# Kernel tuning notes

Measured on AMD Instinct MI355X. Metric: run time of the kernel, lower is better.

## Reference

```python
import jax, jax.numpy as jnp
import numpy as np

WS, SHIFT = 4, 2
Z, H, W = 16, 32, 32
C, HEADS, MLP = 384, 12, 1536
B = 4
N = WS ** 3                      # tokens per 3D window = 64
NW = (Z // WS) * (H // WS) * (W // WS)  # windows per sample = 256
L = Z * H * W
HEAD_DIM = C // HEADS


def _rel_pos_index():
    # replicates meshgrid_3d (which reverses its args) + index arithmetic
    arrs = (np.arange(WS), np.arange(WS), np.arange(WS))  # already symmetric (cubic)
    grids = []
    for i in range(3):
        slc = [1, 1, 1]; slc[i] = WS
        a = arrs[i].reshape(slc)
        for j in range(3):
            if j != i:
                a = a.repeat(WS, axis=j)
        grids.append(a)
    coords = np.stack(grids).reshape(3, -1)            # [3, N]
    rel = coords[:, :, None] - coords[:, None, :]      # [3, N, N]
    rel = rel.transpose(1, 2, 0)                       # [N, N, 3]
    rel[:, :, 0] += WS - 1
    rel[:, :, 1] += WS - 1
    rel[:, :, 2] += WS - 1
    rel[:, :, 0] *= (2 * WS - 1) * (2 * WS - 1)
    rel[:, :, 1] *= 2 * WS - 1
    return rel.sum(-1)                                 # [N, N] ints in [0, (2ws-1)^3)


def _attn_mask():
    # shifted-window mask, exactly as in build()
    m = np.zeros((Z, H, W))
    sl = (slice(0, -WS), slice(-WS, -SHIFT), slice(-SHIFT, None))
    cnt = 0
    for z in sl:
        for h in sl:
            for w in sl:
                m[z, h, w] = cnt
                cnt += 1
    mw = m.reshape(Z // WS, WS, H // WS, WS, W // WS, WS)
    mw = mw.transpose(0, 2, 4, 1, 3, 5).reshape(-1, N)        # [nW, N]
    diff = mw[:, None, :] - mw[:, :, None]                    # [nW, N, N]
    return np.where(diff != 0, -100.0, 0.0).astype(np.float32)


REL_IDX = jnp.asarray(_rel_pos_index())
MASK = jnp.asarray(_attn_mask())


def _ln(x, g, b):
    mu = jnp.mean(x, -1, keepdims=True)
    var = jnp.mean((x - mu) ** 2, -1, keepdims=True)
    return (x - mu) / jnp.sqrt(var + 1e-5) * g + b


def setup_inputs() -> dict:
    key = jax.random.key(0)
    ks = jax.random.split(key, 16)
    s = 0.02
    return {
        "x": jax.random.normal(ks[0], (B, L, C), jnp.float32),
        "norm1_g": jnp.ones((C,), jnp.float32),
        "norm1_b": jnp.zeros((C,), jnp.float32),
        "qkv_w": jax.random.normal(ks[1], (C, 3 * C), jnp.float32) * s,
        "qkv_b": jnp.zeros((3 * C,), jnp.float32),
        "proj_w": jax.random.normal(ks[2], (C, C), jnp.float32) * s,
        "proj_b": jnp.zeros((C,), jnp.float32),
        "rel_bias": jax.random.normal(ks[3], ((2 * WS - 1) ** 3, HEADS), jnp.float32) * s,
        "norm2_g": jnp.ones((C,), jnp.float32),
        "norm2_b": jnp.zeros((C,), jnp.float32),
        "fc1_w": jax.random.normal(ks[4], (C, MLP), jnp.float32) * s,
        "fc1_b": jnp.zeros((MLP,), jnp.float32),
        "fc2_w": jax.random.normal(ks[5], (MLP, C), jnp.float32) * s,
        "fc2_b": jnp.zeros((C,), jnp.float32),
    }


def reference(x, norm1_g, norm1_b, qkv_w, qkv_b, proj_w, proj_b, rel_bias,
              norm2_g, norm2_b, fc1_w, fc1_b, fc2_w, fc2_b):
    b = x.shape[0]
    skip = x
    h = _ln(x, norm1_g, norm1_b).reshape(b, Z, H, W, C)
    h = jnp.roll(h, (-SHIFT, -SHIFT, -SHIFT), axis=(1, 2, 3))
    # window partition -> [b*nW, N, C]
    win = h.reshape(b, Z // WS, WS, H // WS, WS, W // WS, WS, C)
    win = win.transpose(0, 1, 3, 5, 2, 4, 6, 7).reshape(-1, N, C)
    # windowed multi-head attention
    qkv = (win @ qkv_w + qkv_b).reshape(-1, N, 3, HEADS, HEAD_DIM)
    qkv = qkv.transpose(2, 0, 3, 1, 4)                        # [3, bnW, h, N, d]
    q, k, v = qkv[0], qkv[1], qkv[2]
    scale = HEAD_DIM ** -0.5
    attn = jnp.einsum('whnd,whmd->whnm', q * scale, k)        # [bnW, h, N, N]
    bias = rel_bias[REL_IDX.reshape(-1)].reshape(N, N, HEADS).transpose(2, 0, 1)
    attn = attn + bias[None]
    attn = attn.reshape(b, NW, HEADS, N, N) + MASK[None, :, None]
    attn = jax.nn.softmax(attn, axis=-1).reshape(-1, HEADS, N, N)
    o = jnp.einsum('whnm,whmd->whnd', attn, v)
    o = o.transpose(0, 2, 1, 3).reshape(-1, N, C) @ proj_w + proj_b
    # window reverse + unshift
    o = o.reshape(b, Z // WS, H // WS, W // WS, WS, WS, WS, C)
    o = o.transpose(0, 1, 4, 2, 5, 3, 6, 7).reshape(b, Z, H, W, C)
    o = jnp.roll(o, (SHIFT, SHIFT, SHIFT), axis=(1, 2, 3)).reshape(b, L, C)
    x2 = skip + o
    m = _ln(x2, norm2_g, norm2_b)
    m = jax.nn.gelu(m @ fc1_w + fc1_b, approximate=False) @ fc2_w + fc2_b
    return x2 + m
```

## Files before the change

kernel.cpp:

```cpp
#include <hip/hip_runtime.h>
#include <hip/hip_bf16.h>
#include <cstdint>
#include <cmath>


typedef __attribute__((ext_vector_type(4))) float f32x4;
typedef __attribute__((ext_vector_type(8))) __bf16 bf16x8_t;

static __device__ __forceinline__ short f2bf(float f) {
  unsigned u = __builtin_bit_cast(unsigned, f);
  unsigned lsb = (u >> 16) & 1u;
  u += 0x7fffu + lsb;
  return (short)(u >> 16);
}

static __device__ __forceinline__ void gload_lds16(const short* g, short* l) {
  __builtin_amdgcn_global_load_lds(
      (const __attribute__((address_space(1))) void*)g,
      (__attribute__((address_space(3))) void*)l, 16, 0, 0);
}

static constexpr size_t OFF_Q    = 0;
static constexpr size_t OFF_K    = 50331648;
static constexpr size_t OFF_V    = 100663296;
static constexpr size_t OFF_HID  = 0;
static constexpr size_t OFF_WIN  = 201326592;
static constexpr size_t OFF_WQ   = OFF_WIN + 50331648;
static constexpr size_t OFF_WP   = OFF_WQ  + 884736;
static constexpr size_t OFF_W1   = OFF_WP  + 294912;
static constexpr size_t OFF_W2   = OFF_W1  + 1179648;

__global__ void k_w2bf_t(const float* __restrict__ w, short* __restrict__ wt,
                         int K, int N) {
  int idx = blockIdx.x * 256 + threadIdx.x;
  if (idx >= K * N) return;
  int k = idx / N, n = idx - k * N;
  wt[(size_t)n * K + k] = f2bf(w[idx]);
}

__global__ __launch_bounds__(256) void k_ln1_window(
    const float* __restrict__ x, const float* __restrict__ gw,
    const float* __restrict__ gb, short* __restrict__ win) {
  int slot = blockIdx.x * 4 + (threadIdx.x >> 6);
  int lane = threadIdx.x & 63;
  int widx = slot >> 6, n = slot & 63;
  int bidx = widx >> 8, wloc = widx & 255;
  int z = ((wloc >> 6) << 2) + (n >> 4);
  int h = (((wloc >> 3) & 7) << 2) + ((n >> 2) & 3);
  int w = ((wloc & 7) << 2) + (n & 3);
  int zs = (z + 2) & 15, hs = (h + 2) & 31, ws = (w + 2) & 31;
  const float* xp = x + ((size_t)bidx * 16384 + zs * 1024 + hs * 32 + ws) * 384;
  float2 u[3]; float s = 0.f, s2 = 0.f;
#pragma unroll
  for (int j = 0; j < 3; j++) {
    u[j] = *(const float2*)(xp + lane * 2 + j * 128);
    s += u[j].x + u[j].y; s2 += u[j].x * u[j].x + u[j].y * u[j].y;
  }
#pragma unroll
  for (int o = 1; o < 64; o <<= 1) { s += __shfl_xor(s, o); s2 += __shfl_xor(s2, o); }
  float mu = s * (1.f / 384.f);
  float rinv = rsqrtf(s2 * (1.f / 384.f) - mu * mu + 1e-5f);
  short* wp = win + (size_t)slot * 384;
#pragma unroll
  for (int j = 0; j < 3; j++) {
    int c = lane * 2 + j * 128;
    ushort2 o;
    o.x = (unsigned short)f2bf((u[j].x - mu) * rinv * gw[c] + gb[c]);
    o.y = (unsigned short)f2bf((u[j].y - mu) * rinv * gw[c + 1] + gb[c + 1]);
    *(ushort2*)(wp + c) = o;
  }
}

__global__ __launch_bounds__(256) void k_ln2(
    const float* __restrict__ x2, const float* __restrict__ gw,
    const float* __restrict__ gb, short* __restrict__ h2) {
  int t = blockIdx.x * 4 + (threadIdx.x >> 6);
  int lane = threadIdx.x & 63;
  const float* xp = x2 + (size_t)t * 384;
  float2 u[3]; float s = 0.f, s2 = 0.f;
#pragma unroll
  for (int j = 0; j < 3; j++) {
    u[j] = *(const float2*)(xp + lane * 2 + j * 128);
    s += u[j].x + u[j].y; s2 += u[j].x * u[j].x + u[j].y * u[j].y;
  }
#pragma unroll
  for (int o = 1; o < 64; o <<= 1) { s += __shfl_xor(s, o); s2 += __shfl_xor(s2, o); }
  float mu = s * (1.f / 384.f);
  float rinv = rsqrtf(s2 * (1.f / 384.f) - mu * mu + 1e-5f);
  short* hp = h2 + (size_t)t * 384;
#pragma unroll
  for (int j = 0; j < 3; j++) {
    int c = lane * 2 + j * 128;
    ushort2 o;
    o.x = (unsigned short)f2bf((u[j].x - mu) * rinv * gw[c] + gb[c]);
    o.y = (unsigned short)f2bf((u[j].y - mu) * rinv * gw[c + 1] + gb[c + 1]);
    *(ushort2*)(hp + c) = o;
  }
}

template <int EPI, int KDIM>
__global__ __launch_bounds__(256, 2) void k_gemm(
    const short* __restrict__ A, const short* __restrict__ Bt,
    const float* __restrict__ bias, short* __restrict__ ob0,
    short* __restrict__ ob1, short* __restrict__ ob2,
    const float* __restrict__ aux, float* __restrict__ of32) {
  __shared__ short As[24576];
  __shared__ short Bs[12288];
  const int tid = threadIdx.x;
  const int wave = tid >> 6, lane = tid & 63;
  const int g = lane >> 4, li = lane & 15;

  const int nx = gridDim.x;
  const int nwg = nx * gridDim.y;
  int bid = blockIdx.y * nx + blockIdx.x;
  const int cpx = nwg >> 3;
  bid = (bid & 7) * cpx + (bid >> 3);
  const int m0 = (bid / nx) << 8, n0 = (bid % nx) << 7;

  const int u_ = tid >> 3;
  const int s_ = tid & 7;
  const int sx = s_ ^ (u_ & 7);
  const int srow = (u_ << 1) + (sx >> 2);
  const int scol = (sx & 3) << 3;
  const short* gAs = A + (size_t)(m0 + srow) * KDIM + scol;
  const short* gBs = Bt + (size_t)(n0 + srow) * KDIM + scol;
  short* lAs = As + wave * 512;
  short* lBs = Bs + wave * 512;

  const int wm = wave >> 1, wn = wave & 1;
  const int li2 = li >> 1;
  const int slot = (((li & 1) << 2) + g) ^ li2;
  const int abase = wm * 4096 + li2 * 64 + slot * 8;
  const int bbase = wn * 2048 + li2 * 64 + slot * 8;

  f32x4 acc[8][4] = {};

#define STAGE(buf, kt)                                                        \
  do {                                                                        \
    _Pragma("unroll") for (int p = 0; p < 4; p++)                             \
        gload_lds16(gAs + (size_t)(p * 64) * KDIM + (kt),                     \
                    lAs + (buf) * 8192 + p * 2048);                           \
    _Pragma("unroll") for (int p = 0; p < 2; p++)                             \
        gload_lds16(gBs + (size_t)(p * 64) * KDIM + (kt),                     \
                    lBs + (buf) * 4096 + p * 2048);                           \
  } while (0)

#define COMPUTE(buf)                                                          \
  do {                                                                        \
    const short* pa = As + (buf) * 8192 + abase;                              \
    const short* pb = Bs + (buf) * 4096 + bbase;                              \
    bf16x8_t a[8], b[4];                                                      \
    _Pragma("unroll") for (int mi = 0; mi < 8; mi++)                          \
        a[mi] = *(const bf16x8_t*)(pa + mi * 512);                            \
    _Pragma("unroll") for (int ni = 0; ni < 4; ni++)                          \
        b[ni] = *(const bf16x8_t*)(pb + ni * 512);                            \
    _Pragma("unroll") for (int mi = 0; mi < 8; mi++)                          \
        _Pragma("unroll") for (int ni = 0; ni < 4; ni++) acc[mi][ni] =        \
        __builtin_amdgcn_mfma_f32_16x16x32_bf16(a[mi], b[ni], acc[mi][ni],    \
                                                0, 0, 0);                     \
  } while (0)

  constexpr int NT = KDIM / 32;
  STAGE(0, 0);
  STAGE(1, 32);
#pragma unroll 3
  for (int t = 0; t < NT; ++t) {
    asm volatile("s_waitcnt lgkmcnt(0)" ::: "memory");
    __builtin_amdgcn_s_barrier();
    if (t + 2 < NT) {
      STAGE((t + 2) % 3, (t + 2) * 32);
      asm volatile("s_waitcnt vmcnt(12)" ::: "memory");
    } else if (t + 1 < NT) {
      asm volatile("s_waitcnt vmcnt(6)" ::: "memory");
    } else {
      asm volatile("s_waitcnt vmcnt(0)" ::: "memory");
    }
    __builtin_amdgcn_s_barrier();
    COMPUTE(t % 3);
  }
#undef STAGE
#undef COMPUTE

#pragma unroll
  for (int mi = 0; mi < 8; mi++) {
#pragma unroll
    for (int ni = 0; ni < 4; ni++) {
      const int col = n0 + wn * 64 + ni * 16 + li;
      const float bc = bias[col];
      const int rbase = m0 + wm * 128 + mi * 16 + g * 4;
      if constexpr (EPI == 0) {
        const int s = col / 384;
        const int rem = col - s * 384;
        const int head = rem >> 5, d = rem & 31;
#pragma unroll
        for (int r = 0; r < 4; r++) {
          const int row = rbase + r;
          const int widx = row >> 6, n = row & 63;
          float v = acc[mi][ni][r] + bc;
          if (s == 0)
            ob0[(((size_t)widx * 12 + head) * 64 + n) * 32 + d] =
                f2bf(v * 0.17677669529663687f);
          else if (s == 1)
            ob1[(((size_t)widx * 12 + head) * 64 + n) * 32 + d] = f2bf(v);
          else
            ob2[(((size_t)widx * 12 + head) * 32 + d) * 64 + n] = f2bf(v);
        }
      } else if constexpr (EPI == 1) {
#pragma unroll
        for (int r = 0; r < 4; r++) {
          const int row = rbase + r;
          const int widx = row >> 6, n = row & 63;
          const int wloc = widx & 255, bb = widx >> 8;
          const int z = ((wloc >> 6) << 2) + (n >> 4);
          const int h = (((wloc >> 3) & 7) << 2) + ((n >> 2) & 3);
          const int w = ((wloc & 7) << 2) + (n & 3);
          const int zs = (z + 2) & 15, hs = (h + 2) & 31, wsx = (w + 2) & 31;
          const size_t t = (size_t)bb * 16384 + zs * 1024 + hs * 32 + wsx;
          of32[t * 384 + col] = aux[t * 384 + col] + acc[mi][ni][r] + bc;
        }
      } else if constexpr (EPI == 2) {
#pragma unroll
        for (int r = 0; r < 4; r++) {
          const int row = rbase + r;
          float v = acc[mi][ni][r] + bc;
          ob0[(size_t)row * 1536 + col] =
              f2bf(0.5f * v * (1.f + erff(v * 0.70710678118654752f)));
        }
      } else {
#pragma unroll
        for (int r = 0; r < 4; r++) {
          const int row = rbase + r;
          of32[(size_t)row * 384 + col] =
              aux[(size_t)row * 384 + col] + acc[mi][ni][r] + bc;
        }
      }
    }
  }
}

__global__ __launch_bounds__(256) void k_attn(
    const short* __restrict__ qb, const short* __restrict__ kb,
    const short* __restrict__ vb, const float* __restrict__ relb,
    short* __restrict__ owin) {
  __shared__ short pt[4][5120];
  const int wave = threadIdx.x >> 6;
  const int wh_ = blockIdx.x * 4 + wave;
  const int widx = wh_ / 12, head = wh_ - widx * 12;
  const int lane = threadIdx.x & 63;
  const int g = lane >> 4, li = lane & 15;
  const short* qp = qb + (size_t)wh_ * 2048;
  const short* kp = kb + (size_t)wh_ * 2048;
  const short* vp = vb + (size_t)wh_ * 2048;
  short* ptw = pt[wave];
  bf16x8_t kf[4], qf[4];
#pragma unroll
  for (int t = 0; t < 4; t++) {
    kf[t] = *(const bf16x8_t*)(kp + (t * 16 + li) * 32 + g * 8);
    qf[t] = *(const bf16x8_t*)(qp + (t * 16 + li) * 32 + g * 8);
  }
  f32x4 zero = {0.f, 0.f, 0.f, 0.f};
  f32x4 st[4][4];
#pragma unroll
  for (int ti = 0; ti < 4; ti++)
#pragma unroll
    for (int tj = 0; tj < 4; tj++)
      st[ti][tj] = __builtin_amdgcn_mfma_f32_16x16x32_bf16(kf[ti], qf[tj], zero, 0, 0, 0);
  const int wloc = widx & 255;
  const int wz = wloc >> 6, wh2 = (wloc >> 3) & 7, ww2 = wloc & 7;
#pragma unroll
  for (int tj = 0; tj < 4; tj++) {
    const int qn = tj * 16 + li;
    const int qz = qn >> 4, qh = (qn >> 2) & 3, qw = qn & 3;
    const int cq = ((wz < 3) ? 0 : ((qz < 2) ? 1 : 2)) * 9 +
                   ((wh2 < 7) ? 0 : ((qh < 2) ? 1 : 2)) * 3 +
                   ((ww2 < 7) ? 0 : ((qw < 2) ? 1 : 2));
    float mx = -1e30f;
#pragma unroll
    for (int ti = 0; ti < 4; ti++) {
#pragma unroll
      for (int r = 0; r < 4; r++) {
        const int kn = ti * 16 + g * 4 + r;
        const int kz = kn >> 4, kh = (kn >> 2) & 3, kw = kn & 3;
        const int ck = ((wz < 3) ? 0 : ((kz < 2) ? 1 : 2)) * 9 +
                       ((wh2 < 7) ? 0 : ((kh < 2) ? 1 : 2)) * 3 +
                       ((ww2 < 7) ? 0 : ((kw < 2) ? 1 : 2));
        const int idx = (qz - kz + 3) * 49 + (qh - kh + 3) * 7 + (qw - kw + 3);
        float v = st[ti][tj][r] + relb[idx * 12 + head] + ((ck == cq) ? 0.f : -100.f);
        st[ti][tj][r] = v;
        mx = fmaxf(mx, v);
      }
    }
    mx = fmaxf(mx, __shfl_xor(mx, 16));
    mx = fmaxf(mx, __shfl_xor(mx, 32));
    float sum = 0.f;
#pragma unroll
    for (int ti = 0; ti < 4; ti++)
#pragma unroll
      for (int r = 0; r < 4; r++) {
        float e = __expf(st[ti][tj][r] - mx);
        st[ti][tj][r] = e;
        sum += e;
      }
    sum += __shfl_xor(sum, 16);
    sum += __shfl_xor(sum, 32);
    const float rs = 1.f / sum;
#pragma unroll
    for (int ti = 0; ti < 4; ti++)
#pragma unroll
      for (int r = 0; r < 4; r++)
        ptw[qn * 80 + ti * 16 + g * 4 + r] = f2bf(st[ti][tj][r] * rs);
  }
  __syncthreads();
  f32x4 o[4][2] = {};
#pragma unroll
  for (int kb2 = 0; kb2 < 2; kb2++) {
    bf16x8_t pa[4], bv[2];
#pragma unroll
    for (int tq = 0; tq < 4; tq++)
      pa[tq] = *(const bf16x8_t*)(ptw + (tq * 16 + li) * 80 + kb2 * 32 + g * 8);
#pragma unroll
    for (int td = 0; td < 2; td++)
      bv[td] = *(const bf16x8_t*)(vp + (td * 16 + li) * 64 + kb2 * 32 + g * 8);
#pragma unroll
    for (int tq = 0; tq < 4; tq++)
#pragma unroll
      for (int td = 0; td < 2; td++)
        o[tq][td] = __builtin_amdgcn_mfma_f32_16x16x32_bf16(pa[tq], bv[td], o[tq][td], 0, 0, 0);
  }
#pragma unroll
  for (int tq = 0; tq < 4; tq++)
#pragma unroll
    for (int td = 0; td < 2; td++)
#pragma unroll
      for (int r = 0; r < 4; r++) {
        const int qn = tq * 16 + g * 4 + r;
        const int d = td * 16 + li;
        owin[((size_t)widx * 64 + qn) * 384 + head * 32 + d] = f2bf(o[tq][td][r]);
      }
}

extern "C" void kernel_launch(void* const* d_in, const int* in_sizes, int n_in,
                              void* d_out, int out_size, void* d_ws,
                              size_t ws_size, hipStream_t stream) {
  (void)in_sizes; (void)n_in; (void)out_size; (void)ws_size;
  const float* x      = (const float*)d_in[0];
  const float* n1g    = (const float*)d_in[1];
  const float* n1b    = (const float*)d_in[2];
  const float* qkv_w  = (const float*)d_in[3];
  const float* qkv_b  = (const float*)d_in[4];
  const float* proj_w = (const float*)d_in[5];
  const float* proj_b = (const float*)d_in[6];
  const float* relb   = (const float*)d_in[7];
  const float* n2g    = (const float*)d_in[8];
  const float* n2b    = (const float*)d_in[9];
  const float* fc1_w  = (const float*)d_in[10];
  const float* fc1_b  = (const float*)d_in[11];
  const float* fc2_w  = (const float*)d_in[12];
  const float* fc2_b  = (const float*)d_in[13];
  float* out = (float*)d_out;
  char* ws = (char*)d_ws;

  short* qbuf = (short*)(ws + OFF_Q);
  short* kbuf = (short*)(ws + OFF_K);
  short* vbuf = (short*)(ws + OFF_V);
  short* hid  = (short*)(ws + OFF_HID);
  short* win  = (short*)(ws + OFF_WIN);
  short* owin = (short*)(ws + OFF_WIN);
  short* h2   = (short*)(ws + OFF_WIN);
  float* x2   = out;
  short* wq   = (short*)(ws + OFF_WQ);
  short* wp   = (short*)(ws + OFF_WP);
  short* w1   = (short*)(ws + OFF_W1);
  short* w2   = (short*)(ws + OFF_W2);

  k_w2bf_t<<<(384 * 1152 + 255) / 256, 256, 0, stream>>>(qkv_w, wq, 384, 1152);
  k_w2bf_t<<<(384 * 384 + 255) / 256, 256, 0, stream>>>(proj_w, wp, 384, 384);
  k_w2bf_t<<<(384 * 1536 + 255) / 256, 256, 0, stream>>>(fc1_w, w1, 384, 1536);
  k_w2bf_t<<<(1536 * 384 + 255) / 256, 256, 0, stream>>>(fc2_w, w2, 1536, 384);

  k_ln1_window<<<16384, 256, 0, stream>>>(x, n1g, n1b, win);
  k_gemm<0, 384><<<dim3(9, 256), 256, 0, stream>>>(win, wq, qkv_b, qbuf, kbuf,
                                                   vbuf, nullptr, nullptr);
  k_attn<<<3072, 256, 0, stream>>>(qbuf, kbuf, vbuf, relb, owin);
  k_gemm<1, 384><<<dim3(3, 256), 256, 0, stream>>>(owin, wp, proj_b, nullptr,
                                                   nullptr, nullptr, x, x2);
  k_ln2<<<16384, 256, 0, stream>>>(x2, n2g, n2b, h2);
  k_gemm<2, 384><<<dim3(12, 256), 256, 0, stream>>>(h2, w1, fc1_b, hid, nullptr,
                                                    nullptr, nullptr, nullptr);
  k_gemm<3, 1536><<<dim3(3, 256), 256, 0, stream>>>(hid, w2, fc2_b, nullptr,
                                                    nullptr, nullptr, x2, out);
}
```

Measured before the change: 799.0 us.

## Stage QKV and FC1 epilogues through swizzled LDS for vectorized stores; tanh GELU

For the QKV projection and FC1 GEMMs, the epilogue now writes bf16 results into a swizzled shared-memory tile and then emits coalesced 16-byte global stores, instead of scattered 2-byte stores into head-major and transposed-V layouts. The aim is to cut uncoalesced write traffic. FC1's exact erf GELU is replaced by a tanh approximation computed with __expf, which changes numerics slightly. The extra LDS pass adds two barriers and reuses the A/B staging buffers.

```diff
diff --git a/kernel.cpp b/kernel.cpp
--- a/kernel.cpp
+++ b/kernel.cpp
@@ -5,6 +5,7 @@
 
 
 typedef __attribute__((ext_vector_type(4))) float f32x4;
+typedef __attribute__((ext_vector_type(4))) int i32x4;
 typedef __attribute__((ext_vector_type(8))) __bf16 bf16x8_t;
 
 static __device__ __forceinline__ short f2bf(float f) {
@@ -12,6 +13,13 @@
   unsigned lsb = (u >> 16) & 1u;
   u += 0x7fffu + lsb;
   return (short)(u >> 16);
+}
+
+static __device__ __forceinline__ float fgelu(float x) {
+  float u = 0.7978845608028654f * x * (1.f + 0.044715f * x * x);
+  float e = __expf(2.f * u);
+  float t = 1.f - 2.f / (e + 1.f);
+  return 0.5f * x * (1.f + t);
 }
 
 static __device__ __forceinline__ void gload_lds16(const short* g, short* l) {
@@ -104,8 +112,9 @@
     const float* __restrict__ bias, short* __restrict__ ob0,
     short* __restrict__ ob1, short* __restrict__ ob2,
     const float* __restrict__ aux, float* __restrict__ of32) {
-  __shared__ short As[24576];
-  __shared__ short Bs[12288];
+  __shared__ short smem[36864];
+  short* As = smem;
+  short* Bs = smem + 24576;
   const int tid = threadIdx.x;
   const int wave = tid >> 6, lane = tid & 63;
   const int g = lane >> 4, li = lane & 15;
@@ -181,57 +190,102 @@
 #undef STAGE
 #undef COMPUTE
 
-#pragma unroll
-  for (int mi = 0; mi < 8; mi++) {
-#pragma unroll
-    for (int ni = 0; ni < 4; ni++) {
-      const int col = n0 + wn * 64 + ni * 16 + li;
-      const float bc = bias[col];
-      const int rbase = m0 + wm * 128 + mi * 16 + g * 4;
-      if constexpr (EPI == 0) {
-        const int s = col / 384;
-        const int rem = col - s * 384;
-        const int head = rem >> 5, d = rem & 31;
+  if constexpr (EPI == 0 || EPI == 2) {
+    __syncthreads();
+    short* ct = smem;
+    const int s = (EPI == 0) ? (n0 / 384) : 0;
+    const float scale =
+        (EPI == 0 && s == 0) ? 0.17677669529663687f : 1.f;
+#pragma unroll
+    for (int mi = 0; mi < 8; mi++) {
+#pragma unroll
+      for (int ni = 0; ni < 4; ni++) {
+        const int colc = wn * 64 + ni * 16 + li;
+        const float bc = bias[n0 + colc];
 #pragma unroll
         for (int r = 0; r < 4; r++) {
-          const int row = rbase + r;
-          const int widx = row >> 6, n = row & 63;
+          const int row = wm * 128 + mi * 16 + g * 4 + r;
           float v = acc[mi][ni][r] + bc;
-          if (s == 0)
-            ob0[(((size_t)widx * 12 + head) * 64 + n) * 32 + d] =
-                f2bf(v * 0.17677669529663687f);
-          else if (s == 1)
-            ob1[(((size_t)widx * 12 + head) * 64 + n) * 32 + d] = f2bf(v);
-          else
-            ob2[(((size_t)widx * 12 + head) * 32 + d) * 64 + n] = f2bf(v);
+          int idx16, sub;
+          if constexpr (EPI == 0) {
+            const int hh = colc >> 5, d = colc & 31;
+            const int widx_l = row >> 6, n = row & 63;
+            const int run = widx_l * 4 + hh;
+            if (s < 2) {
+              idx16 = run * 256 + n * 4 + (d >> 3);
+              idx16 ^= (idx16 >> 4) & 7;
+              sub = d & 7;
+            } else {
+              idx16 = run * 256 + d * 8 + (n >> 3);
+              idx16 ^= (idx16 >> 3) & 7;
+              sub = n & 7;
+            }
+            v *= scale;
+          } else {
+            idx16 = row * 16 + (colc >> 3);
+            idx16 ^= (idx16 >> 4) & 7;
+            sub = colc & 7;
+            v = fgelu(v);
+          }
+          ct[idx16 * 8 + sub] = f2bf(v);
         }
-      } else if constexpr (EPI == 1) {
-#pragma unroll
-        for (int r = 0; r < 4; r++) {
-          const int row = rbase + r;
-          const int widx = row >> 6, n = row & 63;
-          const int wloc = widx & 255, bb = widx >> 8;
-          const int z = ((wloc >> 6) << 2) + (n >> 4);
-          const int h = (((wloc >> 3) & 7) << 2) + ((n >> 2) & 3);
-          const int w = ((wloc & 7) << 2) + (n & 3);
-          const int zs = (z + 2) & 15, hs = (h + 2) & 31, wsx = (w + 2) & 31;
-          const size_t t = (size_t)bb * 16384 + zs * 1024 + hs * 32 + wsx;
-          of32[t * 384 + col] = aux[t * 384 + col] + acc[mi][ni][r] + bc;
-        }
-      } else if constexpr (EPI == 2) {
-#pragma unroll
-        for (int r = 0; r < 4; r++) {
-          const int row = rbase + r;
-          float v = acc[mi][ni][r] + bc;
-          ob0[(size_t)row * 1536 + col] =
-              f2bf(0.5f * v * (1.f + erff(v * 0.70710678118654752f)));
-        }
-      } else {
-#pragma unroll
-        for (int r = 0; r < 4; r++) {
-          const int row = rbase + r;
-          of32[(size_t)row * 384 + col] =
-              aux[(size_t)row * 384 + col] + acc[mi][ni][r] + bc;
+      }
+    }
+    __syncthreads();
+    if constexpr (EPI == 0) {
+      const int hb = (n0 % 384) >> 5;
+      const int wg0 = m0 >> 6;
+      short* dst = (s == 0) ? ob0 : (s == 1) ? ob1 : ob2;
+#pragma unroll
+      for (int k2 = 0; k2 < 16; k2++) {
+        const int c = k2 * 256 + tid;
+        const int cs = (s < 2) ? (c ^ ((c >> 4) & 7)) : (c ^ ((c >> 3) & 7));
+        i32x4 val = *(const i32x4*)(ct + cs * 8);
+        const int run = c >> 8, sub2 = c & 255;
+        short* gp = dst +
+                    ((size_t)(wg0 + (run >> 2)) * 12 + hb + (run & 3)) * 2048 +
+                    sub2 * 8;
+        *(i32x4*)gp = val;
+      }
+    } else {
+#pragma unroll
+      for (int k2 = 0; k2 < 16; k2++) {
+        const int c = k2 * 256 + tid;
+        const int cs = c ^ ((c >> 4) & 7);
+        i32x4 val = *(const i32x4*)(ct + cs * 8);
+        const int row = c >> 4;
+        short* gp = ob0 + (size_t)(m0 + row) * 1536 + n0 + (c & 15) * 8;
+        *(i32x4*)gp = val;
+      }
+    }
+  } else {
+#pragma unroll
+    for (int mi = 0; mi < 8; mi++) {
+#pragma unroll
+      for (int ni = 0; ni < 4; ni++) {
+        const int col = n0 + wn * 64 + ni * 16 + li;
+        const float bc = bias[col];
+        const int rbase = m0 + wm * 128 + mi * 16 + g * 4;
+        if constexpr (EPI == 1) {
+#pragma unroll
+          for (int r = 0; r < 4; r++) {
+            const int row = rbase + r;
+            const int widx = row >> 6, n = row & 63;
+            const int wloc = widx & 255, bb = widx >> 8;
+            const int z = ((wloc >> 6) << 2) + (n >> 4);
+            const int h = (((wloc >> 3) & 7) << 2) + ((n >> 2) & 3);
+            const int w = ((wloc & 7) << 2) + (n & 3);
+            const int zs = (z + 2) & 15, hs = (h + 2) & 31, wsx = (w + 2) & 31;
+            const size_t t = (size_t)bb * 16384 + zs * 1024 + hs * 32 + wsx;
+            of32[t * 384 + col] = aux[t * 384 + col] + acc[mi][ni][r] + bc;
+          }
+        } else {
+#pragma unroll
+          for (int r = 0; r < 4; r++) {
+            const int row = rbase + r;
+            of32[(size_t)row * 384 + col] =
+                aux[(size_t)row * 384 + col] + acc[mi][ni][r] + bc;
+          }
         }
       }
     }
```

After: 700.5 us. 12.3% less time.
